# Kernel optimization log

Hardware: AMD Instinct MI355X
Metric: run time of the kernel (lower is better)

The kernel has to match this reference:

```python
import jax, jax.numpy as jnp
import numpy as np

B, C, W, H, D = 2, 256, 32, 32, 32
CH = C // 2  # 128
LN_EPS = 1e-5


def _spatial_pool(x, wm, bm):
    # x: [B,C,W,H,D]; wm: [C]; bm: scalar. 1x1x1 conv C->1 == channel dot.
    b, c = x.shape[0], x.shape[1]
    xf = x.reshape(b, c, -1)                       # [B,C,N]
    mask = jnp.einsum('bcn,c->bn', xf, wm) + bm    # [B,N]
    attn = jax.nn.softmax(mask, axis=1)            # softmax over spatial N
    return jnp.einsum('bcn,bn->bc', xf, attn)      # [B,C] weighted-sum pool


def _channel_add(ctx, w1, b1, g, be, w2, b2):
    # 1x1 conv C->C/2, LayerNorm over C/2, ReLU, 1x1 conv C/2->C
    h = ctx @ w1.T + b1                            # [B,CH]
    mu = jnp.mean(h, axis=-1, keepdims=True)
    var = jnp.mean((h - mu) ** 2, axis=-1, keepdims=True)
    h = (h - mu) * jax.lax.rsqrt(var + LN_EPS) * g + be
    h = jax.nn.relu(h)
    return h @ w2.T + b2                           # [B,C]


def setup_inputs() -> dict:
    key = jax.random.key(0)
    ks = jax.random.split(key, 20)
    s = 0.02
    d = {
        'preds_S': jax.random.normal(ks[0], (B, C, W, H, D), jnp.float32),
        'preds_T': jax.random.normal(ks[1], (B, C, W, H, D), jnp.float32),
        'wm_s': jax.random.normal(ks[2], (C,), jnp.float32) * s,
        'bm_s': jnp.zeros((), jnp.float32),
        'wm_t': jax.random.normal(ks[3], (C,), jnp.float32) * s,
        'bm_t': jnp.zeros((), jnp.float32),
        'w1_s': jax.random.normal(ks[4], (CH, C), jnp.float32) * s,
        'b1_s': jnp.zeros((CH,), jnp.float32),
        'g_s': jnp.ones((CH,), jnp.float32),
        'be_s': jnp.zeros((CH,), jnp.float32),
        'w2_s': jax.random.normal(ks[5], (C, CH), jnp.float32) * s,
        'b2_s': jnp.zeros((C,), jnp.float32),
        'w1_t': jax.random.normal(ks[6], (CH, C), jnp.float32) * s,
        'b1_t': jnp.zeros((CH,), jnp.float32),
        'g_t': jnp.ones((CH,), jnp.float32),
        'be_t': jnp.zeros((CH,), jnp.float32),
        'w2_t': jax.random.normal(ks[7], (C, CH), jnp.float32) * s,
        'b2_t': jnp.zeros((C,), jnp.float32),
    }
    return d


def reference(preds_S, preds_T, wm_s, bm_s, wm_t, bm_t,
              w1_s, b1_s, g_s, be_s, w2_s, b2_s,
              w1_t, b1_t, g_t, be_t, w2_t, b2_t):
    ctx_s = _spatial_pool(preds_S, wm_s, bm_s)     # [B,C]
    ctx_t = _spatial_pool(preds_T, wm_t, bm_t)
    add_s = _channel_add(ctx_s, w1_s, b1_s, g_s, be_s, w2_s, b2_s)  # [B,C]
    add_t = _channel_add(ctx_t, w1_t, b1_t, g_t, be_t, w2_t, b2_t)
    out_s = preds_S + add_s[:, :, None, None, None]
    out_t = preds_T + add_t[:, :, None, None, None]
    diff = out_s - out_t
    return jnp.sum(diff * diff) / preds_S.shape[0]
```

## Files before the change

### kernel.cpp

```cpp
#include <hip/hip_runtime.h>
#include <math.h>

#define Bc   2
#define Cc   256
#define Nn   32768
#define CHc  128
#define LN_EPS 1e-5f

#define TN    64
#define TPB   512
#define NQ    16
#define CG    32
#define CPG   8
#define TPBLK 2
#define GRIDX (Nn / (TN * TPBLK))

__global__ __launch_bounds__(TPB) void gc_fused(
    const float* __restrict__ S, const float* __restrict__ T,
    const float* __restrict__ wms, const float* __restrict__ bms,
    const float* __restrict__ wmt, const float* __restrict__ bmt,
    float* __restrict__ ctxnum,
    float* __restrict__ rowsum,
    float* __restrict__ den,
    float* __restrict__ sumsq) {
  const int b   = blockIdx.y;
  const int tid = threadIdx.x;
  const int nq  = tid & (NQ - 1);
  const int cg  = tid >> 4;
  const int c0  = cg * CPG;

  __shared__ float4 mred[2][CG][NQ];
  __shared__ float  cred[Cc * 17];

  float wS[CPG], wT[CPG];
#pragma unroll
  for (int i = 0; i < CPG; ++i) { wS[i] = wms[c0 + i]; wT[i] = wmt[c0 + i]; }
  const float bS = bms[0];
  const float bT = bmt[0];

  float cs[CPG], ct[CPG], rs[CPG];
#pragma unroll
  for (int i = 0; i < CPG; ++i) { cs[i] = 0.f; ct[i] = 0.f; rs[i] = 0.f; }
  float sq = 0.f, pden_s = 0.f, pden_t = 0.f;

  for (int it = 0; it < TPBLK; ++it) {
    const int n0 = (blockIdx.x * TPBLK + it) * TN + nq * 4;
    const float* Sp = S + ((size_t)b * Cc + c0) * Nn + n0;
    const float* Tp = T + ((size_t)b * Cc + c0) * Nn + n0;

    float4 s4[CPG], t4[CPG];
#pragma unroll
    for (int i = 0; i < CPG; ++i) s4[i] = *(const float4*)(Sp + (size_t)i * Nn);
#pragma unroll
    for (int i = 0; i < CPG; ++i) t4[i] = *(const float4*)(Tp + (size_t)i * Nn);

    float4 ms = make_float4(0.f, 0.f, 0.f, 0.f);
    float4 mt = make_float4(0.f, 0.f, 0.f, 0.f);
#pragma unroll
    for (int i = 0; i < CPG; ++i) {
      ms.x += wS[i] * s4[i].x; ms.y += wS[i] * s4[i].y;
      ms.z += wS[i] * s4[i].z; ms.w += wS[i] * s4[i].w;
      mt.x += wT[i] * t4[i].x; mt.y += wT[i] * t4[i].y;
      mt.z += wT[i] * t4[i].z; mt.w += wT[i] * t4[i].w;
      const float dx = s4[i].x - t4[i].x, dy = s4[i].y - t4[i].y;
      const float dz = s4[i].z - t4[i].z, dw = s4[i].w - t4[i].w;
      rs[i] += dx + dy + dz + dw;
      sq += dx * dx + dy * dy + dz * dz + dw * dw;
    }

    __syncthreads();
    mred[0][cg][nq] = ms;
    mred[1][cg][nq] = mt;
    __syncthreads();
#pragma unroll
    for (int st = CG / 2; st > 0; st >>= 1) {
      if (cg < st) {
        const float4 a0 = mred[0][cg][nq], a1 = mred[0][cg + st][nq];
        mred[0][cg][nq] =
            make_float4(a0.x + a1.x, a0.y + a1.y, a0.z + a1.z, a0.w + a1.w);
        const float4 b0 = mred[1][cg][nq], b1 = mred[1][cg + st][nq];
        mred[1][cg][nq] =
            make_float4(b0.x + b1.x, b0.y + b1.y, b0.z + b1.z, b0.w + b1.w);
      }
      __syncthreads();
    }
    const float4 Ms = mred[0][0][nq];
    const float4 Mt = mred[1][0][nq];
    float4 es, et;
    es.x = __expf(Ms.x + bS); es.y = __expf(Ms.y + bS);
    es.z = __expf(Ms.z + bS); es.w = __expf(Ms.w + bS);
    et.x = __expf(Mt.x + bT); et.y = __expf(Mt.y + bT);
    et.z = __expf(Mt.z + bT); et.w = __expf(Mt.w + bT);

    if (cg == 0) {
      pden_s += es.x + es.y + es.z + es.w;
      pden_t += et.x + et.y + et.z + et.w;
    }
#pragma unroll
    for (int i = 0; i < CPG; ++i) {
      cs[i] += s4[i].x * es.x + s4[i].y * es.y + s4[i].z * es.z + s4[i].w * es.w;
      ct[i] += t4[i].x * et.x + t4[i].y * et.y + t4[i].z * et.z + t4[i].w * et.w;
    }
  }

  __syncthreads();
#pragma unroll
  for (int i = 0; i < CPG; ++i) cred[(c0 + i) * 17 + nq] = cs[i];
  __syncthreads();
  if (tid < Cc) {
    float v = 0.f;
#pragma unroll
    for (int k = 0; k < NQ; ++k) v += cred[tid * 17 + k];
    atomicAdd(&ctxnum[((size_t)0 * Bc + b) * Cc + tid], v);
  }
  __syncthreads();
#pragma unroll
  for (int i = 0; i < CPG; ++i) cred[(c0 + i) * 17 + nq] = ct[i];
  __syncthreads();
  if (tid < Cc) {
    float v = 0.f;
#pragma unroll
    for (int k = 0; k < NQ; ++k) v += cred[tid * 17 + k];
    atomicAdd(&ctxnum[((size_t)1 * Bc + b) * Cc + tid], v);
  }
  __syncthreads();
#pragma unroll
  for (int i = 0; i < CPG; ++i) cred[(c0 + i) * 17 + nq] = rs[i];
  __syncthreads();
  if (tid < Cc) {
    float v = 0.f;
#pragma unroll
    for (int k = 0; k < NQ; ++k) v += cred[tid * 17 + k];
    atomicAdd(&rowsum[(size_t)b * Cc + tid], v);
  }
  __syncthreads();
  cred[tid] = sq;
  __syncthreads();
  for (int st = TPB / 2; st > 0; st >>= 1) {
    if (tid < st) cred[tid] += cred[tid + st];
    __syncthreads();
  }
  if (tid == 0) atomicAdd(sumsq, cred[0]);
  __syncthreads();
  if (tid < NQ) { cred[tid] = pden_s; cred[NQ + tid] = pden_t; }
  __syncthreads();
  if (tid == 0) {
    float a = 0.f, c = 0.f;
#pragma unroll
    for (int k = 0; k < NQ; ++k) { a += cred[k]; c += cred[NQ + k]; }
    atomicAdd(&den[0 * Bc + b], a);
    atomicAdd(&den[1 * Bc + b], c);
  }
}

__global__ __launch_bounds__(1024) void gc_k4a_mlp(
    const float* __restrict__ ctxr, const float* __restrict__ den,
    const float* __restrict__ w1s, const float* __restrict__ b1s,
    const float* __restrict__ gs,  const float* __restrict__ bes,
    const float* __restrict__ w2s, const float* __restrict__ b2s,
    const float* __restrict__ w1t, const float* __restrict__ b1t,
    const float* __restrict__ gt,  const float* __restrict__ bet,
    const float* __restrict__ w2t, const float* __restrict__ b2t,
    float* __restrict__ addv) {
  const int tt  = blockIdx.x >> 1;
  const int b   = blockIdx.x & 1;
  const int tid = threadIdx.x;

  const float* w1 = tt ? w1t : w1s;
  const float* b1 = tt ? b1t : b1s;
  const float* g  = tt ? gt  : gs;
  const float* be = tt ? bet : bes;
  const float* w2 = tt ? w2t : w2s;
  const float* b2 = tt ? b2t : b2s;

  __shared__ float cxs[Cc];
  __shared__ float part[1024];
  __shared__ float hbuf[CHc];
  __shared__ float hr[CHc];
  __shared__ float2 red2[128];
  __shared__ float mu_s, rstd_s;

  if (tid < Cc)
    cxs[tid] = ctxr[((size_t)tt * Bc + b) * Cc + tid] / den[tt * Bc + b];
  __syncthreads();

  {
    const int j = tid >> 3, s = tid & 7;
    const float* wr = w1 + j * Cc + s * 32;
    const float4* cx4 = (const float4*)(cxs + s * 32);
    float acc = 0.f;
#pragma unroll
    for (int k = 0; k < 8; ++k) {
      const float4 w = *(const float4*)(wr + k * 4);
      const float4 x = cx4[k];
      acc += w.x * x.x + w.y * x.y + w.z * x.z + w.w * x.w;
    }
    part[tid] = acc;
  }
  __syncthreads();
  if (tid < CHc) {
    float h = b1[tid];
#pragma unroll
    for (int q = 0; q < 8; ++q) h += part[tid * 8 + q];
    hbuf[tid] = h;
  }
  __syncthreads();

  if (tid < CHc) {
    const float v = hbuf[tid];
    red2[tid] = make_float2(v, v * v);
  }
  __syncthreads();
  for (int s = 64; s > 0; s >>= 1) {
    if (tid < s) {
      red2[tid].x += red2[tid + s].x;
      red2[tid].y += red2[tid + s].y;
    }
    __syncthreads();
  }
  if (tid == 0) {
    const float mu = red2[0].x / (float)CHc;
    const float var = red2[0].y / (float)CHc - mu * mu;
    mu_s = mu;
    rstd_s = rsqrtf(var + LN_EPS);
  }
  __syncthreads();
  if (tid < CHc) {
    const float v = (hbuf[tid] - mu_s) * rstd_s * g[tid] + be[tid];
    hr[tid] = v > 0.f ? v : 0.f;
  }
  __syncthreads();

  {
    const int c = tid >> 2, q = tid & 3;
    const float* wr = w2 + c * CHc + q * 32;
    const float4* h4 = (const float4*)(hr + q * 32);
    float acc = 0.f;
#pragma unroll
    for (int k = 0; k < 8; ++k) {
      const float4 w = *(const float4*)(wr + k * 4);
      const float4 x = h4[k];
      acc += w.x * x.x + w.y * x.y + w.z * x.z + w.w * x.w;
    }
    part[tid] = acc;
  }
  __syncthreads();
  if (tid < Cc) {
    float acc = b2[tid];
#pragma unroll
    for (int q = 0; q < 4; ++q) acc += part[tid * 4 + q];
    addv[((size_t)tt * Bc + b) * Cc + tid] = acc;
  }
}

__global__ __launch_bounds__(256) void gc_k4b_final(
    const float* __restrict__ addv, const float* __restrict__ rowsum,
    const float* __restrict__ sumsq, float* __restrict__ out) {
  const int tid = threadIdx.x;
  __shared__ float red[256];
  float part = 0.f;
  for (int job = tid; job < Bc * Cc; job += 256) {
    const int c = job & (Cc - 1);
    const int b = job >> 8;
    const float delta = addv[((size_t)0 * Bc + b) * Cc + c] -
                        addv[((size_t)1 * Bc + b) * Cc + c];
    part += 2.f * delta * rowsum[(size_t)b * Cc + c] +
            (float)Nn * delta * delta;
  }
  red[tid] = part;
  __syncthreads();
  for (int s = 128; s > 0; s >>= 1) {
    if (tid < s) red[tid] += red[tid + s];
    __syncthreads();
  }
  if (tid == 0) out[0] = (red[0] + sumsq[0]) / (float)Bc;
}

extern "C" void kernel_launch(void* const* d_in, const int* in_sizes, int n_in,
                              void* d_out, int out_size, void* d_ws,
                              size_t ws_size, hipStream_t stream) {
  const float* S   = (const float*)d_in[0];
  const float* T   = (const float*)d_in[1];
  const float* wms = (const float*)d_in[2];
  const float* bms = (const float*)d_in[3];
  const float* wmt = (const float*)d_in[4];
  const float* bmt = (const float*)d_in[5];
  const float* w1s = (const float*)d_in[6];
  const float* b1s = (const float*)d_in[7];
  const float* gs  = (const float*)d_in[8];
  const float* bes = (const float*)d_in[9];
  const float* w2s = (const float*)d_in[10];
  const float* b2s = (const float*)d_in[11];
  const float* w1t = (const float*)d_in[12];
  const float* b1t = (const float*)d_in[13];
  const float* gt  = (const float*)d_in[14];
  const float* bet = (const float*)d_in[15];
  const float* w2t = (const float*)d_in[16];
  const float* b2t = (const float*)d_in[17];
  float* out = (float*)d_out;

  float* ws     = (float*)d_ws;
  float* ctxnum = ws;
  float* rowsum = ctxnum + 2 * Bc * Cc;
  float* den    = rowsum + Bc * Cc;
  float* sumsq  = den + 4;
  float* addv   = sumsq + 1;

  hipMemsetAsync(d_ws, 0, (2 * Bc * Cc + Bc * Cc + 4 + 1) * sizeof(float),
                 stream);

  gc_fused<<<dim3(GRIDX, Bc), TPB, 0, stream>>>(S, T, wms, bms, wmt, bmt,
                                                ctxnum, rowsum, den, sumsq);
  gc_k4a_mlp<<<4, 1024, 0, stream>>>(ctxnum, den, w1s, b1s, gs, bes, w2s, b2s,
                                     w1t, b1t, gt, bet, w2t, b2t, addv);
  gc_k4b_final<<<1, 256, 0, stream>>>(addv, rowsum, sumsq, out);
}
```

Before: 207.9 us.

## Replace LDS tree reductions with wave shuffles and one tile per block

Each block now handles a single 64-column tile instead of two, doubling the grid. The channel-group mask reduction and the squared-difference reduction move from shared-memory trees with many barriers to wavefront xor-shuffles plus a small cross-wave pass. The three per-channel reductions share one barrier through separate LDS buffers. This cuts barrier count and serial LDS steps, but doubles the global atomics per channel and raises LDS use, which may reduce occupancy.

New measurement: 208.4 us. About the same (+0.2%).

```diff
diff --git a/kernel.cpp b/kernel.cpp
--- a/kernel.cpp
+++ b/kernel.cpp
@@ -12,8 +12,7 @@
 #define NQ    16
 #define CG    32
 #define CPG   8
-#define TPBLK 2
-#define GRIDX (Nn / (TN * TPBLK))
+#define GRIDX (Nn / TN)
 
 __global__ __launch_bounds__(TPB) void gc_fused(
     const float* __restrict__ S, const float* __restrict__ T,
@@ -23,131 +22,119 @@
     float* __restrict__ rowsum,
     float* __restrict__ den,
     float* __restrict__ sumsq) {
-  const int b   = blockIdx.y;
-  const int tid = threadIdx.x;
-  const int nq  = tid & (NQ - 1);
-  const int cg  = tid >> 4;
-  const int c0  = cg * CPG;
-
-  __shared__ float4 mred[2][CG][NQ];
-  __shared__ float  cred[Cc * 17];
-
-  float wS[CPG], wT[CPG];
-#pragma unroll
-  for (int i = 0; i < CPG; ++i) { wS[i] = wms[c0 + i]; wT[i] = wmt[c0 + i]; }
+  const int b    = blockIdx.y;
+  const int tid  = threadIdx.x;
+  const int nq   = tid & (NQ - 1);
+  const int cg   = tid >> 4;
+  const int wv   = tid >> 6;
+  const int lane = tid & 63;
+  const int c0   = cg * CPG;
+  const int n0   = blockIdx.x * TN + nq * 4;
+
+  __shared__ float4 mredw[2][8][NQ];
+  __shared__ float  credA[Cc * 17];
+  __shared__ float  credB[Cc * 17];
+  __shared__ float  credC[Cc * 17];
+  __shared__ float  sqred[8];
+  __shared__ float  denred[2][NQ];
+
   const float bS = bms[0];
   const float bT = bmt[0];
 
-  float cs[CPG], ct[CPG], rs[CPG];
-#pragma unroll
-  for (int i = 0; i < CPG; ++i) { cs[i] = 0.f; ct[i] = 0.f; rs[i] = 0.f; }
-  float sq = 0.f, pden_s = 0.f, pden_t = 0.f;
-
-  for (int it = 0; it < TPBLK; ++it) {
-    const int n0 = (blockIdx.x * TPBLK + it) * TN + nq * 4;
-    const float* Sp = S + ((size_t)b * Cc + c0) * Nn + n0;
-    const float* Tp = T + ((size_t)b * Cc + c0) * Nn + n0;
-
-    float4 s4[CPG], t4[CPG];
-#pragma unroll
-    for (int i = 0; i < CPG; ++i) s4[i] = *(const float4*)(Sp + (size_t)i * Nn);
-#pragma unroll
-    for (int i = 0; i < CPG; ++i) t4[i] = *(const float4*)(Tp + (size_t)i * Nn);
-
-    float4 ms = make_float4(0.f, 0.f, 0.f, 0.f);
-    float4 mt = make_float4(0.f, 0.f, 0.f, 0.f);
-#pragma unroll
-    for (int i = 0; i < CPG; ++i) {
-      ms.x += wS[i] * s4[i].x; ms.y += wS[i] * s4[i].y;
-      ms.z += wS[i] * s4[i].z; ms.w += wS[i] * s4[i].w;
-      mt.x += wT[i] * t4[i].x; mt.y += wT[i] * t4[i].y;
-      mt.z += wT[i] * t4[i].z; mt.w += wT[i] * t4[i].w;
-      const float dx = s4[i].x - t4[i].x, dy = s4[i].y - t4[i].y;
-      const float dz = s4[i].z - t4[i].z, dw = s4[i].w - t4[i].w;
-      rs[i] += dx + dy + dz + dw;
-      sq += dx * dx + dy * dy + dz * dz + dw * dw;
+  const float* Sp = S + ((size_t)b * Cc + c0) * Nn + n0;
+  const float* Tp = T + ((size_t)b * Cc + c0) * Nn + n0;
+
+  float4 s4[CPG], t4[CPG];
+#pragma unroll
+  for (int i = 0; i < CPG; ++i) s4[i] = *(const float4*)(Sp + (size_t)i * Nn);
+#pragma unroll
+  for (int i = 0; i < CPG; ++i) t4[i] = *(const float4*)(Tp + (size_t)i * Nn);
+
+  float wS[CPG], wT[CPG];
+#pragma unroll
+  for (int i = 0; i < CPG; ++i) { wS[i] = wms[c0 + i]; wT[i] = wmt[c0 + i]; }
+
+  float4 ms = make_float4(0.f, 0.f, 0.f, 0.f);
+  float4 mt = make_float4(0.f, 0.f, 0.f, 0.f);
+  float rs[CPG];
+  float sq = 0.f;
+#pragma unroll
+  for (int i = 0; i < CPG; ++i) {
+    ms.x += wS[i] * s4[i].x; ms.y += wS[i] * s4[i].y;
+    ms.z += wS[i] * s4[i].z; ms.w += wS[i] * s4[i].w;
+    mt.x += wT[i] * t4[i].x; mt.y += wT[i] * t4[i].y;
+    mt.z += wT[i] * t4[i].z; mt.w += wT[i] * t4[i].w;
+    const float dx = s4[i].x - t4[i].x, dy = s4[i].y - t4[i].y;
+    const float dz = s4[i].z - t4[i].z, dw = s4[i].w - t4[i].w;
+    rs[i] = dx + dy + dz + dw;
+    sq += dx * dx + dy * dy + dz * dz + dw * dw;
+  }
+
+#pragma unroll
+  for (int m = 16; m <= 32; m <<= 1) {
+    ms.x += __shfl_xor(ms.x, m); ms.y += __shfl_xor(ms.y, m);
+    ms.z += __shfl_xor(ms.z, m); ms.w += __shfl_xor(ms.w, m);
+    mt.x += __shfl_xor(mt.x, m); mt.y += __shfl_xor(mt.y, m);
+    mt.z += __shfl_xor(mt.z, m); mt.w += __shfl_xor(mt.w, m);
+  }
+  if (lane < NQ) { mredw[0][wv][nq] = ms; mredw[1][wv][nq] = mt; }
+
+#pragma unroll
+  for (int m = 1; m < 64; m <<= 1) sq += __shfl_xor(sq, m);
+  if (lane == 0) sqred[wv] = sq;
+
+  __syncthreads();
+
+  float4 Ms = make_float4(0.f, 0.f, 0.f, 0.f);
+  float4 Mt = make_float4(0.f, 0.f, 0.f, 0.f);
+#pragma unroll
+  for (int w = 0; w < 8; ++w) {
+    const float4 a = mredw[0][w][nq];
+    Ms.x += a.x; Ms.y += a.y; Ms.z += a.z; Ms.w += a.w;
+    const float4 c = mredw[1][w][nq];
+    Mt.x += c.x; Mt.y += c.y; Mt.z += c.z; Mt.w += c.w;
+  }
+  float4 es, et;
+  es.x = __expf(Ms.x + bS); es.y = __expf(Ms.y + bS);
+  es.z = __expf(Ms.z + bS); es.w = __expf(Ms.w + bS);
+  et.x = __expf(Mt.x + bT); et.y = __expf(Mt.y + bT);
+  et.z = __expf(Mt.z + bT); et.w = __expf(Mt.w + bT);
+
+  if (tid < NQ) {
+    denred[0][tid] = es.x + es.y + es.z + es.w;
+    denred[1][tid] = et.x + et.y + et.z + et.w;
+  }
+
+#pragma unroll
+  for (int i = 0; i < CPG; ++i) {
+    credA[(c0 + i) * 17 + nq] =
+        s4[i].x * es.x + s4[i].y * es.y + s4[i].z * es.z + s4[i].w * es.w;
+    credB[(c0 + i) * 17 + nq] =
+        t4[i].x * et.x + t4[i].y * et.y + t4[i].z * et.z + t4[i].w * et.w;
+    credC[(c0 + i) * 17 + nq] = rs[i];
+  }
+  __syncthreads();
+
+  if (tid < Cc) {
+    float a = 0.f, c = 0.f, r = 0.f;
+#pragma unroll
+    for (int k = 0; k < NQ; ++k) {
+      a += credA[tid * 17 + k];
+      c += credB[tid * 17 + k];
+      r += credC[tid * 17 + k];
     }
-
-    __syncthreads();
-    mred[0][cg][nq] = ms;
-    mred[1][cg][nq] = mt;
-    __syncthreads();
-#pragma unroll
-    for (int st = CG / 2; st > 0; st >>= 1) {
-      if (cg < st) {
-        const float4 a0 = mred[0][cg][nq], a1 = mred[0][cg + st][nq];
-        mred[0][cg][nq] =
-            make_float4(a0.x + a1.x, a0.y + a1.y, a0.z + a1.z, a0.w + a1.w);
-        const float4 b0 = mred[1][cg][nq], b1 = mred[1][cg + st][nq];
-        mred[1][cg][nq] =
-            make_float4(b0.x + b1.x, b0.y + b1.y, b0.z + b1.z, b0.w + b1.w);
-      }
-      __syncthreads();
-    }
-    const float4 Ms = mred[0][0][nq];
-    const float4 Mt = mred[1][0][nq];
-    float4 es, et;
-    es.x = __expf(Ms.x + bS); es.y = __expf(Ms.y + bS);
-    es.z = __expf(Ms.z + bS); es.w = __expf(Ms.w + bS);
-    et.x = __expf(Mt.x + bT); et.y = __expf(Mt.y + bT);
-    et.z = __expf(Mt.z + bT); et.w = __expf(Mt.w + bT);
-
-    if (cg == 0) {
-      pden_s += es.x + es.y + es.z + es.w;
-      pden_t += et.x + et.y + et.z + et.w;
-    }
-#pragma unroll
-    for (int i = 0; i < CPG; ++i) {
-      cs[i] += s4[i].x * es.x + s4[i].y * es.y + s4[i].z * es.z + s4[i].w * es.w;
-      ct[i] += t4[i].x * et.x + t4[i].y * et.y + t4[i].z * et.z + t4[i].w * et.w;
-    }
-  }
-
-  __syncthreads();
-#pragma unroll
-  for (int i = 0; i < CPG; ++i) cred[(c0 + i) * 17 + nq] = cs[i];
-  __syncthreads();
-  if (tid < Cc) {
+    atomicAdd(&ctxnum[((size_t)0 * Bc + b) * Cc + tid], a);
+    atomicAdd(&ctxnum[((size_t)1 * Bc + b) * Cc + tid], c);
+    atomicAdd(&rowsum[(size_t)b * Cc + tid], r);
+  } else if (tid == Cc) {
     float v = 0.f;
 #pragma unroll
-    for (int k = 0; k < NQ; ++k) v += cred[tid * 17 + k];
-    atomicAdd(&ctxnum[((size_t)0 * Bc + b) * Cc + tid], v);
-  }
-  __syncthreads();
-#pragma unroll
-  for (int i = 0; i < CPG; ++i) cred[(c0 + i) * 17 + nq] = ct[i];
-  __syncthreads();
-  if (tid < Cc) {
-    float v = 0.f;
-#pragma unroll
-    for (int k = 0; k < NQ; ++k) v += cred[tid * 17 + k];
-    atomicAdd(&ctxnum[((size_t)1 * Bc + b) * Cc + tid], v);
-  }
-  __syncthreads();
-#pragma unroll
-  for (int i = 0; i < CPG; ++i) cred[(c0 + i) * 17 + nq] = rs[i];
-  __syncthreads();
-  if (tid < Cc) {
-    float v = 0.f;
-#pragma unroll
-    for (int k = 0; k < NQ; ++k) v += cred[tid * 17 + k];
-    atomicAdd(&rowsum[(size_t)b * Cc + tid], v);
-  }
-  __syncthreads();
-  cred[tid] = sq;
-  __syncthreads();
-  for (int st = TPB / 2; st > 0; st >>= 1) {
-    if (tid < st) cred[tid] += cred[tid + st];
-    __syncthreads();
-  }
-  if (tid == 0) atomicAdd(sumsq, cred[0]);
-  __syncthreads();
-  if (tid < NQ) { cred[tid] = pden_s; cred[NQ + tid] = pden_t; }
-  __syncthreads();
-  if (tid == 0) {
+    for (int w = 0; w < 8; ++w) v += sqred[w];
+    atomicAdd(sumsq, v);
+  } else if (tid == Cc + 1) {
     float a = 0.f, c = 0.f;
 #pragma unroll
-    for (int k = 0; k < NQ; ++k) { a += cred[k]; c += cred[NQ + k]; }
+    for (int k = 0; k < NQ; ++k) { a += denred[0][k]; c += denred[1][k]; }
     atomicAdd(&den[0 * Bc + b], a);
     atomicAdd(&den[1 * Bc + b], c);
   }
```
